# Kernel tuning notes

Hardware: AMD Instinct MI355X
Metric: run time of the kernel (lower is better)

Reference implementation:

```python
import jax, jax.numpy as jnp
import numpy as np

C = 256
C4 = C // 4  # 64
B = 4
N = 4096
FACTOR = float(np.sqrt(C4))


def setup_inputs() -> dict:
    key = jax.random.key(0)
    k1, k2, k3, k4 = jax.random.split(key, 4)
    x = jax.random.normal(k1, (B, C, N), dtype=jnp.float32)
    # q_conv and k_conv share the SAME weight (tied in the torch module)
    W_qk = jax.random.normal(k2, (C4, C), dtype=jnp.float32) * (1.0 / np.sqrt(C))
    W_v = jax.random.normal(k3, (C4, C), dtype=jnp.float32) * (1.0 / np.sqrt(C))
    b_v = jax.random.normal(k4, (C4,), dtype=jnp.float32) * 0.01
    return {"x": x, "W_qk": W_qk, "W_v": W_v, "b_v": b_v}


def reference(x, W_qk, W_v, b_v):
    # Conv1d with kernel size 1 == per-position linear: [B,C,N] -> [B,C4,N]
    x_q = jnp.einsum('oc,bcn->bon', W_qk, x)          # [B, C4, N]
    x_k = x_q                                          # tied weights: k == q
    x_v = jnp.einsum('oc,bcn->bon', W_v, x) + b_v[None, :, None]  # [B, C4, N]
    # energy = x_k.permute(0,2,1) @ x_q : [B, N, N]
    energy = jnp.einsum('bcn,bcm->bnm', x_k, x_q) / FACTOR
    attention = jax.nn.softmax(energy, axis=-1)        # softmax over last dim
    x_r = jnp.einsum('bcn,bnm->bcm', x_v, attention)   # [B, C4, N]
    return x_r
```

## Files before the change

### kernel.cpp

```cpp
#include <hip/hip_runtime.h>


#define CC 256
#define C4C 64
#define NBATCH 4
#define NN 4096
#define QSCALE 0.42466089f
#define SHIFT2 12.0f

typedef _Float16 f16;
typedef _Float16 half2v __attribute__((ext_vector_type(2)));
typedef _Float16 half4 __attribute__((ext_vector_type(4)));
typedef _Float16 half8 __attribute__((ext_vector_type(8)));
typedef __fp16 fp16x2 __attribute__((ext_vector_type(2)));
typedef float floatx4 __attribute__((ext_vector_type(4)));

static __device__ __forceinline__ half2v pkrtz(float a, float b) {
  fp16x2 r = __builtin_amdgcn_cvt_pkrtz(a, b);
  return __builtin_bit_cast(half2v, r);
}

#define LOADQ(T, A0, A1)                                                   \
  { const f16* p_ = Qb + (size_t)(T) * 1024 + l * 8;                       \
    A0 = *(const half8*)(p_); A1 = *(const half8*)(p_ + 512); }

#define XT_PITCH 264
__global__ __launch_bounds__(256) void qv_kernel(
    const float* __restrict__ x, const float* __restrict__ Wqk,
    const float* __restrict__ Wv, const float* __restrict__ bv,
    f16* __restrict__ Qtb, f16* __restrict__ V4)
{
  __shared__ __align__(16) f16 xt[32][XT_PITCH];
  const int b = blockIdx.y;
  const int n0 = blockIdx.x * 32;
  const int tid = threadIdx.x;

  {
    const int nq = tid & 7;
    const int cb = tid >> 3;
    const int c = cb * 8;
    const float* xp = x + (size_t)b * CC * NN + n0 + nq * 4;
    float4 r[8];
#pragma unroll
    for (int j = 0; j < 8; ++j)
      r[j] = *(const float4*)(xp + (size_t)(c + j) * NN);
#pragma unroll
    for (int s = 0; s < 4; ++s) {
      half8 h;
#pragma unroll
      for (int j = 0; j < 8; ++j) h[j] = (f16)(((const float*)&r[j])[s]);
      *(half8*)(&xt[nq * 4 + s][c]) = h;
    }
  }

  const int w = tid >> 6, l = tid & 63, lr = l & 15, lg = l >> 4;
  const float* Wsrc = (w < 2) ? Wqk : Wv;
  const int ocb = (w & 1) * 32;
  half8 af[2][8];
#pragma unroll
  for (int t = 0; t < 2; ++t) {
    const float* wp = Wsrc + (size_t)(ocb + t * 16 + lr) * CC + 8 * lg;
#pragma unroll
    for (int kk = 0; kk < 8; ++kk) {
      float4 wa = *(const float4*)(wp + kk * 32);
      float4 wb = *(const float4*)(wp + kk * 32 + 4);
      half8 h;
      h[0] = (f16)wa.x; h[1] = (f16)wa.y; h[2] = (f16)wa.z; h[3] = (f16)wa.w;
      h[4] = (f16)wb.x; h[5] = (f16)wb.y; h[6] = (f16)wb.z; h[7] = (f16)wb.w;
      af[t][kk] = h;
    }
  }

  __syncthreads();

  floatx4 acc[2][2] = {{{0.f,0.f,0.f,0.f},{0.f,0.f,0.f,0.f}},
                       {{0.f,0.f,0.f,0.f},{0.f,0.f,0.f,0.f}}};
#pragma unroll
  for (int nt = 0; nt < 2; ++nt) {
#pragma unroll
    for (int kk = 0; kk < 8; ++kk) {
      half8 bf = *(const half8*)(&xt[nt * 16 + lr][kk * 32 + 8 * lg]);
      acc[0][nt] = __builtin_amdgcn_mfma_f32_16x16x32_f16(af[0][kk], bf, acc[0][nt], 0, 0, 0);
      acc[1][nt] = __builtin_amdgcn_mfma_f32_16x16x32_f16(af[1][kk], bf, acc[1][nt], 0, 0, 0);
    }
  }

  if (w < 2) {
#pragma unroll
    for (int t = 0; t < 2; ++t)
#pragma unroll
      for (int nt = 0; nt < 2; ++nt) {
        int T = (n0 >> 4) + nt;
        int kg = 2 * t + (lg >> 1);
        union { f16 h[4]; unsigned long long u; } q4;
#pragma unroll
        for (int i = 0; i < 4; ++i) q4.h[i] = (f16)(acc[t][nt][i] * QSCALE);
        *(unsigned long long*)(Qtb + (size_t)(b * 256 + T) * 1024 + w * 512
                               + (kg * 16 + lr) * 8 + (lg & 1) * 4) = q4.u;
      }
  } else {
#pragma unroll
    for (int t = 0; t < 2; ++t)
#pragma unroll
      for (int nt = 0; nt < 2; ++nt) {
        int T = (n0 >> 4) + nt;
        int oc = (w - 2) * 32 + t * 16 + 4 * lg;
#pragma unroll
        for (int i = 0; i < 4; ++i)
          V4[(size_t)(b * 256 + T) * 1024 + (oc + i) * 16 + lr] =
              (f16)(acc[t][nt][i] + bv[oc + i]);
      }
  }
}

__global__ __launch_bounds__(512) void z_kernel(
    const f16* __restrict__ Qtb, float* __restrict__ Zinv)
{
  __shared__ float zl[8][64];
  const int bx = blockIdx.x;
  const int xcd = bx & 7, slot = bx >> 3;
  const int b = xcd >> 1;
  const int wu = ((xcd & 1) << 5) | slot;
  const int n0t = wu * 4;
  const int tid = threadIdx.x;
  const int w = tid >> 6, l = tid & 63, lr = l & 15, lg = l >> 4;
  const f16* Qb = Qtb + (size_t)b * 256 * 1024;

  half8 a[4][2];
#pragma unroll
  for (int t = 0; t < 4; ++t) LOADQ(n0t + t, a[t][0], a[t][1]);

  const int tstr = w * 32;
  float rs[4][4];
#pragma unroll
  for (int t = 0; t < 4; ++t)
#pragma unroll
    for (int i = 0; i < 4; ++i) rs[t][i] = 0.f;

#pragma unroll 1
  for (int ch = 0; ch < 4; ++ch) {
    half8 bb[8][2];
#pragma unroll
    for (int mt = 0; mt < 8; ++mt) {
      const f16* p_ = Qb + (size_t)(tstr + ch * 8 + mt) * 1024 + l * 8;
      bb[mt][0] = *(const half8*)(p_);
      bb[mt][1] = *(const half8*)(p_ + 512);
    }
#pragma unroll
    for (int mt = 0; mt < 8; ++mt) {
      floatx4 d[4];
#pragma unroll
      for (int t = 0; t < 4; ++t) {
        d[t] = (floatx4){0.f, 0.f, 0.f, 0.f};
        d[t] = __builtin_amdgcn_mfma_f32_16x16x32_f16(a[t][0], bb[mt][0], d[t], 0, 0, 0);
        d[t] = __builtin_amdgcn_mfma_f32_16x16x32_f16(a[t][1], bb[mt][1], d[t], 0, 0, 0);
      }
#pragma unroll
      for (int t = 0; t < 4; ++t)
#pragma unroll
        for (int i = 0; i < 4; ++i)
          rs[t][i] += __builtin_amdgcn_exp2f(d[t][i]);
    }
  }

#pragma unroll
  for (int t = 0; t < 4; ++t)
#pragma unroll
    for (int i = 0; i < 4; ++i) {
      float v = rs[t][i];
      v += __shfl_xor(v, 1); v += __shfl_xor(v, 2);
      v += __shfl_xor(v, 4); v += __shfl_xor(v, 8);
      rs[t][i] = v;
    }
  if (lr == 0) {
#pragma unroll
    for (int t = 0; t < 4; ++t)
#pragma unroll
      for (int i = 0; i < 4; ++i)
        zl[w][16 * t + 4 * lg + i] = rs[t][i];
  }
  __syncthreads();
  if (tid < 64) {
    float s = 0.f;
#pragma unroll
    for (int ww = 0; ww < 8; ++ww) s += zl[ww][tid];
    Zinv[b * NN + n0t * 16 + tid] = 4096.0f / s;
  }
}

#define LOADV(NB, UA)                                                      \
  { const f16* up_ = Vb + (size_t)(NB) * 1024 + 4 * lg;                    \
    _Pragma("unroll")                                                      \
    for (int cs = 0; cs < 4; ++cs)                                         \
      UA[cs] = *(const half4*)(up_ + (16 * cs + lr) * 16); }

__global__ __launch_bounds__(512, 4) void av_kernel(
    const f16* __restrict__ Qtb, const f16* __restrict__ V4,
    const float* __restrict__ Zinv, float* __restrict__ Out)
{
  __shared__ float red[8][2][16][17];

  const int bx = blockIdx.x;
  const int xcd = bx & 7, slot = bx >> 3;
  const int b = xcd >> 1;
  const int m0 = (((xcd & 1) << 6) | slot) * 32;
  const int tid = threadIdx.x;
  const int w = tid >> 6;
  const int l = tid & 63;
  const int lr = l & 15, lg = l >> 4;

  const f16* Qb = Qtb + (size_t)b * 256 * 1024;
  const f16* Vb = V4 + (size_t)b * 256 * 1024;
  const float* Zb = Zinv + b * NN;

  half8 bq[2][2];
  LOADQ((m0 >> 4), bq[0][0], bq[0][1]);
  LOADQ((m0 >> 4) + 1, bq[1][0], bq[1][1]);

  floatx4 o[4][2];
#pragma unroll
  for (int cs = 0; cs < 4; ++cs)
#pragma unroll
    for (int t = 0; t < 2; ++t) o[cs][t] = (floatx4){0.f, 0.f, 0.f, 0.f};

#pragma unroll 2
  for (int it = 0; it < 32; ++it) {
    const int T = it * 8 + w;
    half8 a0, a1;
    LOADQ(T, a0, a1);
    half4 va[4];
    LOADV(T, va);
    const float4 zi = *(const float4*)(Zb + T * 16 + 4 * lg);

    floatx4 dA = {-SHIFT2, -SHIFT2, -SHIFT2, -SHIFT2};
    floatx4 dB = {-SHIFT2, -SHIFT2, -SHIFT2, -SHIFT2};
    dA = __builtin_amdgcn_mfma_f32_16x16x32_f16(a0, bq[0][0], dA, 0, 0, 0);
    dB = __builtin_amdgcn_mfma_f32_16x16x32_f16(a0, bq[1][0], dB, 0, 0, 0);
    dA = __builtin_amdgcn_mfma_f32_16x16x32_f16(a1, bq[0][1], dA, 0, 0, 0);
    dB = __builtin_amdgcn_mfma_f32_16x16x32_f16(a1, bq[1][1], dB, 0, 0, 0);

    half2v p0a = pkrtz(__builtin_amdgcn_exp2f(dA[0]) * zi.x,
                       __builtin_amdgcn_exp2f(dA[1]) * zi.y);
    half2v p0b = pkrtz(__builtin_amdgcn_exp2f(dA[2]) * zi.z,
                       __builtin_amdgcn_exp2f(dA[3]) * zi.w);
    half2v p1a = pkrtz(__builtin_amdgcn_exp2f(dB[0]) * zi.x,
                       __builtin_amdgcn_exp2f(dB[1]) * zi.y);
    half2v p1b = pkrtz(__builtin_amdgcn_exp2f(dB[2]) * zi.z,
                       __builtin_amdgcn_exp2f(dB[3]) * zi.w);
    half4 bt0 = {p0a[0], p0a[1], p0b[0], p0b[1]};
    half4 bt1 = {p1a[0], p1a[1], p1b[0], p1b[1]};
#pragma unroll
    for (int cs = 0; cs < 4; ++cs) {
      o[cs][0] = __builtin_amdgcn_mfma_f32_16x16x16f16(va[cs], bt0, o[cs][0], 0, 0, 0);
      o[cs][1] = __builtin_amdgcn_mfma_f32_16x16x16f16(va[cs], bt1, o[cs][1], 0, 0, 0);
    }
  }

#pragma unroll 1
  for (int cs = 0; cs < 4; ++cs) {
    __syncthreads();
#pragma unroll
    for (int t = 0; t < 2; ++t)
#pragma unroll
      for (int i = 0; i < 4; ++i)
        red[w][t][4 * lg + i][lr] = o[cs][t][i];
    __syncthreads();
    const int t = tid >> 8;
    const int r = (tid >> 4) & 15;
    const int col = tid & 15;
    float ssum = 0.f;
#pragma unroll
    for (int ww = 0; ww < 8; ++ww) ssum += red[ww][t][r][col];
    Out[((size_t)b * C4C + cs * 16 + r) * NN + m0 + t * 16 + col] = ssum;
  }
}

extern "C" void kernel_launch(void* const* d_in, const int* in_sizes, int n_in,
                              void* d_out, int out_size, void* d_ws, size_t ws_size,
                              hipStream_t stream)
{
  const float* x   = (const float*)d_in[0];
  const float* Wqk = (const float*)d_in[1];
  const float* Wv  = (const float*)d_in[2];
  const float* bv  = (const float*)d_in[3];
  float* out = (float*)d_out;

  char* ws = (char*)d_ws;
  f16*   Qtb  = (f16*)(ws);
  f16*   V4   = (f16*)(ws + (2u << 20));
  float* Zinv = (float*)(ws + (4u << 20));

  qv_kernel<<<dim3(128, 4), 256, 0, stream>>>(x, Wqk, Wv, bv, Qtb, V4);
  z_kernel<<<dim3(256), 512, 0, stream>>>(Qtb, Zinv);
  av_kernel<<<dim3(512), 512, 0, stream>>>(Qtb, V4, Zinv, out);
}
```

Before: 60.50 us.

## Fuse three kernels into one cooperative kernel with grid syncs

Merges the QV projection, softmax-normaliser and attention-times-V kernels into a single cooperative launch of 512 blocks, separated by grid-wide barriers, with an XCD-aware block-to-work mapping. The aim is to remove two kernel launch gaps and tail effects and keep data in the L2 of each XCD. In exchange, grid sync costs and idle blocks are added during the Z phase, which uses only half the grid, and the launch falls back to the three-kernel path if the cooperative launch fails.

```diff
diff --git a/kernel.cpp b/kernel.cpp
--- a/kernel.cpp
+++ b/kernel.cpp
@@ -1,4 +1,5 @@
 #include <hip/hip_runtime.h>
+#include <hip/hip_cooperative_groups.h>
 
 
 #define CC 256
@@ -8,6 +9,8 @@
 #define QSCALE 0.42466089f
 #define SHIFT2 12.0f
 
+namespace cg = cooperative_groups;
+
 typedef _Float16 f16;
 typedef _Float16 half2v __attribute__((ext_vector_type(2)));
 typedef _Float16 half4 __attribute__((ext_vector_type(4)));
@@ -25,6 +28,236 @@
     A0 = *(const half8*)(p_); A1 = *(const half8*)(p_ + 512); }
 
 #define XT_PITCH 264
+
+__global__ __launch_bounds__(512, 4) void fused_kernel(
+    const float* __restrict__ x, const float* __restrict__ Wqk,
+    const float* __restrict__ Wv, const float* __restrict__ bv,
+    f16* __restrict__ Qtb, f16* __restrict__ V4,
+    float* __restrict__ Zinv, float* __restrict__ Out)
+{
+  __shared__ __align__(16) f16 xt[32][XT_PITCH];
+  __shared__ float zl[8][64];
+  __shared__ float red[8][2][16][17];
+
+  const int bx = blockIdx.x;
+  const int xcd = bx & 7, slot = bx >> 3;
+  const int b = xcd >> 1;
+  const int tid = threadIdx.x;
+  const int w = tid >> 6, l = tid & 63, lr = l & 15, lg = l >> 4;
+
+  {
+    const int wu = ((xcd & 1) << 6) | slot;
+    const int n0 = wu * 32;
+    {
+      const int nq = tid & 7;
+      const int cb = tid >> 3;
+      const int c = cb * 4;
+      const float* xp = x + (size_t)b * CC * NN + n0 + nq * 4;
+      float4 r[4];
+#pragma unroll
+      for (int j = 0; j < 4; ++j)
+        r[j] = *(const float4*)(xp + (size_t)(c + j) * NN);
+#pragma unroll
+      for (int s = 0; s < 4; ++s) {
+        half4 h;
+#pragma unroll
+        for (int j = 0; j < 4; ++j) h[j] = (f16)(((const float*)&r[j])[s]);
+        *(half4*)(&xt[nq * 4 + s][c]) = h;
+      }
+    }
+    const float* Wsrc = (w < 4) ? Wqk : Wv;
+    const int oc16 = (w & 3) * 16;
+    half8 af[8];
+    {
+      const float* wp = Wsrc + (size_t)(oc16 + lr) * CC + 8 * lg;
+#pragma unroll
+      for (int kk = 0; kk < 8; ++kk) {
+        float4 wa = *(const float4*)(wp + kk * 32);
+        float4 wb = *(const float4*)(wp + kk * 32 + 4);
+        half8 h;
+        h[0] = (f16)wa.x; h[1] = (f16)wa.y; h[2] = (f16)wa.z; h[3] = (f16)wa.w;
+        h[4] = (f16)wb.x; h[5] = (f16)wb.y; h[6] = (f16)wb.z; h[7] = (f16)wb.w;
+        af[kk] = h;
+      }
+    }
+    __syncthreads();
+    floatx4 acc[2] = {{0.f,0.f,0.f,0.f},{0.f,0.f,0.f,0.f}};
+#pragma unroll
+    for (int nt = 0; nt < 2; ++nt)
+#pragma unroll
+      for (int kk = 0; kk < 8; ++kk) {
+        half8 bf = *(const half8*)(&xt[nt * 16 + lr][kk * 32 + 8 * lg]);
+        acc[nt] = __builtin_amdgcn_mfma_f32_16x16x32_f16(af[kk], bf, acc[nt], 0, 0, 0);
+      }
+    if (w < 4) {
+#pragma unroll
+      for (int nt = 0; nt < 2; ++nt) {
+        int T = (n0 >> 4) + nt;
+        int kg = 2 * (w & 1) + (lg >> 1);
+        union { f16 h[4]; unsigned long long u; } q4;
+#pragma unroll
+        for (int i = 0; i < 4; ++i) q4.h[i] = (f16)(acc[nt][i] * QSCALE);
+        *(unsigned long long*)(Qtb + (size_t)(b * 256 + T) * 1024 + (w >> 1) * 512
+                               + (kg * 16 + lr) * 8 + (lg & 1) * 4) = q4.u;
+      }
+    } else {
+#pragma unroll
+      for (int nt = 0; nt < 2; ++nt) {
+        int T = (n0 >> 4) + nt;
+        int oc = oc16 + 4 * lg;
+#pragma unroll
+        for (int i = 0; i < 4; ++i)
+          V4[(size_t)(b * 256 + T) * 1024 + (oc + i) * 16 + lr] =
+              (f16)(acc[nt][i] + bv[oc + i]);
+      }
+    }
+  }
+  cg::this_grid().sync();
+
+  if (bx < 256) {
+    const int xcd2 = bx & 7, slot2 = bx >> 3;
+    const int b2 = xcd2 >> 1;
+    const int wu2 = ((xcd2 & 1) << 5) | slot2;
+    const int n0t = wu2 * 4;
+    const f16* Qb = Qtb + (size_t)b2 * 256 * 1024;
+
+    half8 a[4][2];
+#pragma unroll
+    for (int t = 0; t < 4; ++t) LOADQ(n0t + t, a[t][0], a[t][1]);
+
+    const int tstr = w * 32;
+    float rs[4][4];
+#pragma unroll
+    for (int t = 0; t < 4; ++t)
+#pragma unroll
+      for (int i = 0; i < 4; ++i) rs[t][i] = 0.f;
+
+#pragma unroll 1
+    for (int ch = 0; ch < 4; ++ch) {
+      half8 bb[8][2];
+#pragma unroll
+      for (int mt = 0; mt < 8; ++mt) {
+        const f16* p_ = Qb + (size_t)(tstr + ch * 8 + mt) * 1024 + l * 8;
+        bb[mt][0] = *(const half8*)(p_);
+        bb[mt][1] = *(const half8*)(p_ + 512);
+      }
+#pragma unroll
+      for (int mt = 0; mt < 8; ++mt) {
+        floatx4 d[4];
+#pragma unroll
+        for (int t = 0; t < 4; ++t) {
+          d[t] = (floatx4){0.f, 0.f, 0.f, 0.f};
+          d[t] = __builtin_amdgcn_mfma_f32_16x16x32_f16(a[t][0], bb[mt][0], d[t], 0, 0, 0);
+          d[t] = __builtin_amdgcn_mfma_f32_16x16x32_f16(a[t][1], bb[mt][1], d[t], 0, 0, 0);
+        }
+#pragma unroll
+        for (int t = 0; t < 4; ++t)
+#pragma unroll
+          for (int i = 0; i < 4; ++i)
+            rs[t][i] += __builtin_amdgcn_exp2f(d[t][i]);
+      }
+    }
+
+#pragma unroll
+    for (int t = 0; t < 4; ++t)
+#pragma unroll
+      for (int i = 0; i < 4; ++i) {
+        float v = rs[t][i];
+        v += __shfl_xor(v, 1); v += __shfl_xor(v, 2);
+        v += __shfl_xor(v, 4); v += __shfl_xor(v, 8);
+        rs[t][i] = v;
+      }
+    if (lr == 0) {
+#pragma unroll
+      for (int t = 0; t < 4; ++t)
+#pragma unroll
+        for (int i = 0; i < 4; ++i)
+          zl[w][16 * t + 4 * lg + i] = rs[t][i];
+    }
+    __syncthreads();
+    if (tid < 64) {
+      float s = 0.f;
+#pragma unroll
+      for (int ww = 0; ww < 8; ++ww) s += zl[ww][tid];
+      Zinv[b2 * NN + n0t * 16 + tid] = 4096.0f / s;
+    }
+  }
+  cg::this_grid().sync();
+
+  {
+    const int m0 = (((xcd & 1) << 6) | slot) * 32;
+    const f16* Qb = Qtb + (size_t)b * 256 * 1024;
+    const f16* Vb = V4 + (size_t)b * 256 * 1024;
+    const float* Zb = Zinv + b * NN;
+
+    half8 bq[2][2];
+    LOADQ((m0 >> 4), bq[0][0], bq[0][1]);
+    LOADQ((m0 >> 4) + 1, bq[1][0], bq[1][1]);
+
+    floatx4 o[4][2];
+#pragma unroll
+    for (int cs = 0; cs < 4; ++cs)
+#pragma unroll
+      for (int t = 0; t < 2; ++t) o[cs][t] = (floatx4){0.f, 0.f, 0.f, 0.f};
+
+#pragma unroll 2
+    for (int it = 0; it < 32; ++it) {
+      const int T = it * 8 + w;
+      half8 a0, a1;
+      LOADQ(T, a0, a1);
+      half4 va[4];
+      {
+        const f16* up_ = Vb + (size_t)T * 1024 + 4 * lg;
+#pragma unroll
+        for (int cs = 0; cs < 4; ++cs)
+          va[cs] = *(const half4*)(up_ + (16 * cs + lr) * 16);
+      }
+      const float4 zi = *(const float4*)(Zb + T * 16 + 4 * lg);
+
+      floatx4 dA = {-SHIFT2, -SHIFT2, -SHIFT2, -SHIFT2};
+      floatx4 dB = {-SHIFT2, -SHIFT2, -SHIFT2, -SHIFT2};
+      dA = __builtin_amdgcn_mfma_f32_16x16x32_f16(a0, bq[0][0], dA, 0, 0, 0);
+      dB = __builtin_amdgcn_mfma_f32_16x16x32_f16(a0, bq[1][0], dB, 0, 0, 0);
+      dA = __builtin_amdgcn_mfma_f32_16x16x32_f16(a1, bq[0][1], dA, 0, 0, 0);
+      dB = __builtin_amdgcn_mfma_f32_16x16x32_f16(a1, bq[1][1], dB, 0, 0, 0);
+
+      half2v p0a = pkrtz(__builtin_amdgcn_exp2f(dA[0]) * zi.x,
+                         __builtin_amdgcn_exp2f(dA[1]) * zi.y);
+      half2v p0b = pkrtz(__builtin_amdgcn_exp2f(dA[2]) * zi.z,
+                         __builtin_amdgcn_exp2f(dA[3]) * zi.w);
+      half2v p1a = pkrtz(__builtin_amdgcn_exp2f(dB[0]) * zi.x,
+                         __builtin_amdgcn_exp2f(dB[1]) * zi.y);
+      half2v p1b = pkrtz(__builtin_amdgcn_exp2f(dB[2]) * zi.z,
+                         __builtin_amdgcn_exp2f(dB[3]) * zi.w);
+      half4 bt0 = {p0a[0], p0a[1], p0b[0], p0b[1]};
+      half4 bt1 = {p1a[0], p1a[1], p1b[0], p1b[1]};
+#pragma unroll
+      for (int cs = 0; cs < 4; ++cs) {
+        o[cs][0] = __builtin_amdgcn_mfma_f32_16x16x16f16(va[cs], bt0, o[cs][0], 0, 0, 0);
+        o[cs][1] = __builtin_amdgcn_mfma_f32_16x16x16f16(va[cs], bt1, o[cs][1], 0, 0, 0);
+      }
+    }
+
+#pragma unroll 1
+    for (int cs = 0; cs < 4; ++cs) {
+      __syncthreads();
+#pragma unroll
+      for (int t = 0; t < 2; ++t)
+#pragma unroll
+        for (int i = 0; i < 4; ++i)
+          red[w][t][4 * lg + i][lr] = o[cs][t][i];
+      __syncthreads();
+      const int t = tid >> 8;
+      const int r = (tid >> 4) & 15;
+      const int col = tid & 15;
+      float ssum = 0.f;
+#pragma unroll
+      for (int ww = 0; ww < 8; ++ww) ssum += red[ww][t][r][col];
+      Out[((size_t)b * C4C + cs * 16 + r) * NN + m0 + t * 16 + col] = ssum;
+    }
+  }
+}
+
 __global__ __launch_bounds__(256) void qv_kernel(
     const float* __restrict__ x, const float* __restrict__ Wqk,
     const float* __restrict__ Wv, const float* __restrict__ bv,
@@ -290,7 +523,14 @@
   f16*   V4   = (f16*)(ws + (2u << 20));
   float* Zinv = (float*)(ws + (4u << 20));
 
-  qv_kernel<<<dim3(128, 4), 256, 0, stream>>>(x, Wqk, Wv, bv, Qtb, V4);
-  z_kernel<<<dim3(256), 512, 0, stream>>>(Qtb, Zinv);
-  av_kernel<<<dim3(512), 512, 0, stream>>>(Qtb, V4, Zinv, out);
+  void* args[] = {(void*)&x, (void*)&Wqk, (void*)&Wv, (void*)&bv,
+                  (void*)&Qtb, (void*)&V4, (void*)&Zinv, (void*)&out};
+  hipError_t rc = hipLaunchCooperativeKernel((const void*)fused_kernel,
+                                             dim3(512), dim3(512),
+                                             args, 0, stream);
+  if (rc != hipSuccess) {
+    qv_kernel<<<dim3(128, 4), 256, 0, stream>>>(x, Wqk, Wv, bv, Qtb, V4);
+    z_kernel<<<dim3(256), 512, 0, stream>>>(Qtb, Zinv);
+    av_kernel<<<dim3(512), 512, 0, stream>>>(Qtb, V4, Zinv, out);
+  }
 }
```

New measurement: 199.3 us. 3.29x slower.
